# Optimization experiments

Hardware: AMD Instinct MI355X
Metric: run time of the kernel (lower is better)

Reference implementation:

```python
import jax, jax.numpy as jnp
import numpy as np

N = 50000
E = 800000
IN_FEAT = 128
HIDDEN = 64
HEADS = 4
CLASSES = 40
NEG_SLOPE = 0.2


def setup_inputs() -> dict:
    key = jax.random.key(0)
    ks = jax.random.split(key, 12)
    x = jax.random.normal(ks[0], (N, IN_FEAT), dtype=jnp.float32)
    # edge_index without self loops (module removes then re-adds them)
    src = jax.random.randint(ks[1], (E,), 0, N)
    off = jax.random.randint(ks[2], (E,), 1, N)
    dst = (src + off) % N  # guaranteed dst != src
    edge_index = jnp.stack([src, dst]).astype(jnp.int64)
    g = 1.0 / np.sqrt(IN_FEAT)
    lin1_w = jax.random.normal(ks[3], (IN_FEAT, HEADS * HIDDEN), dtype=jnp.float32) * g
    lin1_b = jax.random.normal(ks[4], (HEADS * HIDDEN,), dtype=jnp.float32) * 0.01
    att1 = jax.random.normal(ks[5], (1, HEADS, 2 * HIDDEN), dtype=jnp.float32) * (1.0 / np.sqrt(2 * HIDDEN))
    bias1 = jnp.zeros((HEADS * HIDDEN,), dtype=jnp.float32)
    lin2_w = jax.random.normal(ks[6], (HEADS * HIDDEN, CLASSES), dtype=jnp.float32) * (1.0 / np.sqrt(HEADS * HIDDEN))
    lin2_b = jax.random.normal(ks[7], (CLASSES,), dtype=jnp.float32) * 0.01
    att2 = jax.random.normal(ks[8], (1, 1, 2 * CLASSES), dtype=jnp.float32) * (1.0 / np.sqrt(2 * CLASSES))
    bias2 = jnp.zeros((CLASSES,), dtype=jnp.float32)
    return {"x": x, "edge_index": edge_index, "lin1_w": lin1_w, "lin1_b": lin1_b,
            "att1": att1, "bias1": bias1, "lin2_w": lin2_w, "lin2_b": lin2_b,
            "att2": att2, "bias2": bias2}


def gat_conv(x, src, dst, W, b_lin, att, bias, heads, oc):
    n = x.shape[0]
    fea = (x @ W + b_lin).reshape(n, heads, oc)            # [N, H, C]
    # attention logits: (cat([x_i, x_j]) * att).sum(-1) decomposed per node
    score_i = jnp.einsum('nhc,hc->nh', fea, att[0, :, :oc])  # target half
    score_j = jnp.einsum('nhc,hc->nh', fea, att[0, :, oc:])  # source half
    alpha = score_i[dst] + score_j[src]                    # [E, H]
    alpha = jax.nn.leaky_relu(alpha, NEG_SLOPE)
    # segment softmax over target node
    amax = jax.ops.segment_max(alpha, dst, num_segments=n)
    alpha = jnp.exp(alpha - amax[dst])
    asum = jax.ops.segment_sum(alpha, dst, num_segments=n)
    alpha = alpha / (asum[dst] + 1e-16)
    # message = x_j * alpha; scatter-add to target
    msg = fea[src] * alpha[:, :, None]                     # [E, H, C]
    out = jax.ops.segment_sum(msg, dst, num_segments=n)
    return out.reshape(n, heads * oc) + bias               # concat=True


def reference(x, edge_index, lin1_w, lin1_b, att1, bias1, lin2_w, lin2_b, att2, bias2):
    n = x.shape[0]
    loop = jnp.arange(n, dtype=edge_index.dtype)
    src = jnp.concatenate([edge_index[0], loop])  # add self loops
    dst = jnp.concatenate([edge_index[1], loop])
    h = gat_conv(x, src, dst, lin1_w, lin1_b, att1, bias1, HEADS, HIDDEN)
    h = jax.nn.relu(h)
    h = gat_conv(h, src, dst, lin2_w, lin2_b, att2, bias2, 1, CLASSES)
    return jax.nn.softmax(h, axis=1)
```

## Files before the change

### kernel.cpp

```cpp
#include <hip/hip_runtime.h>
#include <hip/hip_fp16.h>

#define NN 50000
#define NE 800000
#define INFEAT 128
#define F1 256
#define HID 64
#define CLS 40
#define NEGS 0.2f
#define NB 49

__device__ __forceinline__ float lrelu(float x) { return x > 0.0f ? x : NEGS * x; }

struct alignas(8) H4 { __half2 a, b; };
struct alignas(16) H8 { __half2 a, b, c, d; };

typedef __attribute__((ext_vector_type(8))) _Float16 f16x8;
typedef __attribute__((ext_vector_type(4))) float f32x4;

#define GBM 128
__global__ __launch_bounds__(256) void gemm1_k(const float* __restrict__ A,
                                               const float* __restrict__ W,
                                               const float* __restrict__ b,
                                               const float* __restrict__ att1,
                                               __half* __restrict__ feah,
                                               float* __restrict__ sI,
                                               float* __restrict__ sJ) {
    __shared__ __align__(16) _Float16 As[128][40];
    __shared__ __align__(16) _Float16 Ws[64][40];
    int tid = threadIdx.x;
    int wid = tid >> 6, lane = tid & 63;
    int row0 = blockIdx.x * GBM;
    int head = blockIdx.y;
    int colB = head * 64;
    int lr = lane & 15;
    int lg = lane >> 4;

    f32x4 acc[2][4];
    #pragma unroll
    for (int rt = 0; rt < 2; ++rt)
        #pragma unroll
        for (int ct = 0; ct < 4; ++ct) acc[rt][ct] = (f32x4){0.f, 0.f, 0.f, 0.f};

    int wcol = tid & 63;
    int wkg  = tid >> 6;

    for (int k0 = 0; k0 < INFEAT; k0 += 32) {
        #pragma unroll
        for (int i = 0; i < 4; ++i) {
            int q = tid + 256 * i;
            int r = q >> 3;
            int c4 = (q & 7) * 4;
            int grow = row0 + r;
            float4 v = make_float4(0.f, 0.f, 0.f, 0.f);
            if (grow < NN) v = *(const float4*)&A[(size_t)grow * INFEAT + k0 + c4];
            As[r][c4 + 0] = (_Float16)v.x; As[r][c4 + 1] = (_Float16)v.y;
            As[r][c4 + 2] = (_Float16)v.z; As[r][c4 + 3] = (_Float16)v.w;
        }
        {
            f16x8 wv;
            #pragma unroll
            for (int j = 0; j < 8; ++j)
                wv[j] = (_Float16)W[(size_t)(k0 + wkg * 8 + j) * F1 + colB + wcol];
            *(f16x8*)&Ws[wcol][wkg * 8] = wv;
        }
        __syncthreads();
        f16x8 afrag[2], bfrag[4];
        #pragma unroll
        for (int rt = 0; rt < 2; ++rt)
            afrag[rt] = *(const f16x8*)&As[wid * 32 + rt * 16 + lr][lg * 8];
        #pragma unroll
        for (int ct = 0; ct < 4; ++ct)
            bfrag[ct] = *(const f16x8*)&Ws[ct * 16 + lr][lg * 8];
        #pragma unroll
        for (int rt = 0; rt < 2; ++rt)
            #pragma unroll
            for (int ct = 0; ct < 4; ++ct)
                acc[rt][ct] = __builtin_amdgcn_mfma_f32_16x16x32_f16(
                    afrag[rt], bfrag[ct], acc[rt][ct], 0, 0, 0);
        __syncthreads();
    }
    float aIv[4], aJv[4], bv[4];
    #pragma unroll
    for (int ct = 0; ct < 4; ++ct) {
        int cin = ct * 16 + lr;
        aIv[ct] = att1[head * 2 * HID + cin];
        aJv[ct] = att1[head * 2 * HID + HID + cin];
        bv[ct]  = b[colB + cin];
    }
    #pragma unroll
    for (int rt = 0; rt < 2; ++rt) {
        #pragma unroll
        for (int i = 0; i < 4; ++i) {
            int grow = row0 + wid * 32 + rt * 16 + lg * 4 + i;
            float o[4];
            float sIp = 0.f, sJp = 0.f;
            #pragma unroll
            for (int ct = 0; ct < 4; ++ct) {
                o[ct] = acc[rt][ct][i] + bv[ct];
                sIp += o[ct] * aIv[ct];
                sJp += o[ct] * aJv[ct];
            }
            #pragma unroll
            for (int off = 1; off < 16; off <<= 1) {
                sIp += __shfl_xor(sIp, off);
                sJp += __shfl_xor(sJp, off);
            }
            if (grow < NN) {
                #pragma unroll
                for (int ct = 0; ct < 4; ++ct)
                    feah[(size_t)grow * F1 + colB + ct * 16 + lr] = __float2half(o[ct]);
                if (lr == 0) {
                    sI[grow * 4 + head] = sIp;
                    sJ[grow * 4 + head] = sJp;
                }
            }
        }
    }
}

__global__ void hist_k(const int* __restrict__ dst, int* __restrict__ deg,
                       int* __restrict__ ord) {
    int e = blockIdx.x * blockDim.x + threadIdx.x;
    if (e < NE) ord[e] = atomicAdd(&deg[dst[e]], 1);
}

__global__ __launch_bounds__(1024) void scan1_k(const int* __restrict__ deg,
                                                int* __restrict__ row_off,
                                                int* __restrict__ bsum) {
    __shared__ int tmp[1024];
    int tid = threadIdx.x;
    int gid = blockIdx.x * 1024 + tid;
    int v = (gid < NN) ? deg[gid] : 0;
    tmp[tid] = v;
    __syncthreads();
    #pragma unroll
    for (int off = 1; off < 1024; off <<= 1) {
        int t = (tid >= off) ? tmp[tid - off] : 0;
        __syncthreads();
        tmp[tid] += t;
        __syncthreads();
    }
    if (gid < NN) row_off[gid] = tmp[tid] - v;
    if (tid == 1023) bsum[blockIdx.x] = tmp[1023];
}

__global__ void scan2_k(const int* __restrict__ bsum, int* __restrict__ bpref) {
    int tid = threadIdx.x;
    int orig = (tid < NB) ? bsum[tid] : 0;
    int v = orig;
    #pragma unroll
    for (int off = 1; off < 64; off <<= 1) {
        int t = __shfl_up(v, off);
        if (tid >= off) v += t;
    }
    if (tid < NB) bpref[tid] = v - orig;
}

__global__ __launch_bounds__(1024) void scan3_k(int* __restrict__ row_off,
                                                const int* __restrict__ bpref) {
    int gid = blockIdx.x * 1024 + threadIdx.x;
    if (gid < NN) row_off[gid] += bpref[blockIdx.x];
    if (gid == 0) row_off[NN] = NE;
}

__global__ void scatter_k(const int* __restrict__ src, const int* __restrict__ dst,
                          const int* __restrict__ ord, const int* __restrict__ row_off,
                          const float* __restrict__ sI, const float* __restrict__ sJ,
                          int* __restrict__ csr, float4* __restrict__ ep4) {
    int e = blockIdx.x * blockDim.x + threadIdx.x;
    if (e >= NE) return;
    int s = src[e], d = dst[e];
    int pos = row_off[d] + ord[e];
    float4 si = *(const float4*)&sI[d * 4];
    float4 sj = *(const float4*)&sJ[s * 4];
    float4 r;
    r.x = __expf(lrelu(si.x + sj.x));
    r.y = __expf(lrelu(si.y + sj.y));
    r.z = __expf(lrelu(si.z + sj.z));
    r.w = __expf(lrelu(si.w + sj.w));
    csr[pos] = s;
    ep4[pos] = r;
}

__global__ __launch_bounds__(256, 6) void agg1_k(const __half* __restrict__ feah,
                                                 const float* __restrict__ sI,
                                                 const float* __restrict__ sJ,
                                                 const float* __restrict__ epf,
                                                 const int* __restrict__ row_off,
                                                 const int* __restrict__ csr,
                                                 const float* __restrict__ bias,
                                                 float* __restrict__ out) {
    int wid = threadIdx.x >> 6, lane = threadIdx.x & 63;
    int n = blockIdx.x * 4 + wid;
    if (n >= NN) return;
    int h = lane >> 4;
    int c = lane * 4;
    float p = __expf(lrelu(sI[n * 4 + h] + sJ[n * 4 + h]));
    float asum = p;
    H4 vs = *(const H4*)&feah[(size_t)n * F1 + c];
    float2 sx = __half22float2(vs.a), sy = __half22float2(vs.b);
    float4 acc = make_float4(sx.x * p, sx.y * p, sy.x * p, sy.y * p);
    int beg = row_off[n], end = row_off[n + 1];
    int e = beg;
    for (; e + 8 <= end; e += 8) {
        int s0 = csr[e + 0], s1 = csr[e + 1], s2 = csr[e + 2], s3 = csr[e + 3];
        int s4 = csr[e + 4], s5 = csr[e + 5], s6 = csr[e + 6], s7 = csr[e + 7];
        float p0 = epf[(e + 0) * 4 + h], p1 = epf[(e + 1) * 4 + h];
        float p2 = epf[(e + 2) * 4 + h], p3 = epf[(e + 3) * 4 + h];
        float p4 = epf[(e + 4) * 4 + h], p5 = epf[(e + 5) * 4 + h];
        float p6 = epf[(e + 6) * 4 + h], p7 = epf[(e + 7) * 4 + h];
        H4 v0 = *(const H4*)&feah[(size_t)s0 * F1 + c];
        H4 v1 = *(const H4*)&feah[(size_t)s1 * F1 + c];
        H4 v2 = *(const H4*)&feah[(size_t)s2 * F1 + c];
        H4 v3 = *(const H4*)&feah[(size_t)s3 * F1 + c];
        H4 v4 = *(const H4*)&feah[(size_t)s4 * F1 + c];
        H4 v5 = *(const H4*)&feah[(size_t)s5 * F1 + c];
        H4 v6 = *(const H4*)&feah[(size_t)s6 * F1 + c];
        H4 v7 = *(const H4*)&feah[(size_t)s7 * F1 + c];
        asum += ((p0 + p1) + (p2 + p3)) + ((p4 + p5) + (p6 + p7));
        float2 x0 = __half22float2(v0.a), y0 = __half22float2(v0.b);
        float2 x1 = __half22float2(v1.a), y1 = __half22float2(v1.b);
        float2 x2 = __half22float2(v2.a), y2 = __half22float2(v2.b);
        float2 x3 = __half22float2(v3.a), y3 = __half22float2(v3.b);
        float2 x4 = __half22float2(v4.a), y4 = __half22float2(v4.b);
        float2 x5 = __half22float2(v5.a), y5 = __half22float2(v5.b);
        float2 x6 = __half22float2(v6.a), y6 = __half22float2(v6.b);
        float2 x7 = __half22float2(v7.a), y7 = __half22float2(v7.b);
        acc.x += (x0.x * p0 + x1.x * p1 + x2.x * p2 + x3.x * p3)
               + (x4.x * p4 + x5.x * p5 + x6.x * p6 + x7.x * p7);
        acc.y += (x0.y * p0 + x1.y * p1 + x2.y * p2 + x3.y * p3)
               + (x4.y * p4 + x5.y * p5 + x6.y * p6 + x7.y * p7);
        acc.z += (y0.x * p0 + y1.x * p1 + y2.x * p2 + y3.x * p3)
               + (y4.x * p4 + y5.x * p5 + y6.x * p6 + y7.x * p7);
        acc.w += (y0.y * p0 + y1.y * p1 + y2.y * p2 + y3.y * p3)
               + (y4.y * p4 + y5.y * p5 + y6.y * p6 + y7.y * p7);
    }
    for (; e + 4 <= end; e += 4) {
        int s0 = csr[e], s1 = csr[e + 1], s2 = csr[e + 2], s3 = csr[e + 3];
        float p0 = epf[(e + 0) * 4 + h], p1 = epf[(e + 1) * 4 + h];
        float p2 = epf[(e + 2) * 4 + h], p3 = epf[(e + 3) * 4 + h];
        H4 v0 = *(const H4*)&feah[(size_t)s0 * F1 + c];
        H4 v1 = *(const H4*)&feah[(size_t)s1 * F1 + c];
        H4 v2 = *(const H4*)&feah[(size_t)s2 * F1 + c];
        H4 v3 = *(const H4*)&feah[(size_t)s3 * F1 + c];
        asum += (p0 + p1) + (p2 + p3);
        float2 x0 = __half22float2(v0.a), y0 = __half22float2(v0.b);
        float2 x1 = __half22float2(v1.a), y1 = __half22float2(v1.b);
        float2 x2 = __half22float2(v2.a), y2 = __half22float2(v2.b);
        float2 x3 = __half22float2(v3.a), y3 = __half22float2(v3.b);
        acc.x += x0.x * p0 + x1.x * p1 + x2.x * p2 + x3.x * p3;
        acc.y += x0.y * p0 + x1.y * p1 + x2.y * p2 + x3.y * p3;
        acc.z += y0.x * p0 + y1.x * p1 + y2.x * p2 + y3.x * p3;
        acc.w += y0.y * p0 + y1.y * p1 + y2.y * p2 + y3.y * p3;
    }
    for (; e < end; ++e) {
        int s = csr[e];
        float pe = epf[e * 4 + h];
        asum += pe;
        H4 v = *(const H4*)&feah[(size_t)s * F1 + c];
        float2 x = __half22float2(v.a), y = __half22float2(v.b);
        acc.x += x.x * pe; acc.y += x.y * pe;
        acc.z += y.x * pe; acc.w += y.y * pe;
    }
    float inv = 1.0f / (asum + 1e-16f);
    float4 bv = *(const float4*)&bias[c];
    float4 o;
    o.x = fmaxf(acc.x * inv + bv.x, 0.f);
    o.y = fmaxf(acc.y * inv + bv.y, 0.f);
    o.z = fmaxf(acc.z * inv + bv.z, 0.f);
    o.w = fmaxf(acc.w * inv + bv.w, 0.f);
    *(float4*)&out[(size_t)n * F1 + c] = o;
}

#define G2N 102
__global__ __launch_bounds__(256) void gemm2_k(const float* __restrict__ h1,
                                               const float* __restrict__ W2,
                                               const float* __restrict__ b2,
                                               const float* __restrict__ att2,
                                               __half* __restrict__ fea2h,
                                               float* __restrict__ s2I,
                                               float* __restrict__ s2J) {
    __shared__ float Ws[F1 * CLS];
    __shared__ float redI[G2N][5];
    __shared__ float redJ[G2N][5];
    int tid = threadIdx.x;
    for (int i = tid * 4; i < F1 * CLS; i += 256 * 4)
        *(float4*)&Ws[i] = *(const float4*)&W2[i];
    __syncthreads();
    int nl = tid / 5, g = tid - nl * 5;
    int na = blockIdx.x * G2N + nl * 2;
    int nb = na + 1;
    bool actA = (tid < 255) && (na < NN);
    bool actB = (tid < 255) && (nb < NN);
    int c0 = g * 8;
    float accA[8] = {}, accB[8] = {};
    if (actA) {
        const float* rowA = h1 + (size_t)na * F1;
        const float* rowB = h1 + (size_t)(actB ? nb : na) * F1;
        for (int k = 0; k < F1; k += 4) {
            float4 ha = *(const float4*)&rowA[k];
            float4 hb = *(const float4*)&rowB[k];
            float a[4] = {ha.x, ha.y, ha.z, ha.w};
            float bl[4] = {hb.x, hb.y, hb.z, hb.w};
            #pragma unroll
            for (int kk = 0; kk < 4; ++kk) {
                float4 w0 = *(const float4*)&Ws[(k + kk) * CLS + c0];
                float4 w1 = *(const float4*)&Ws[(k + kk) * CLS + c0 + 4];
                accA[0] += a[kk] * w0.x; accA[1] += a[kk] * w0.y;
                accA[2] += a[kk] * w0.z; accA[3] += a[kk] * w0.w;
                accA[4] += a[kk] * w1.x; accA[5] += a[kk] * w1.y;
                accA[6] += a[kk] * w1.z; accA[7] += a[kk] * w1.w;
                accB[0] += bl[kk] * w0.x; accB[1] += bl[kk] * w0.y;
                accB[2] += bl[kk] * w0.z; accB[3] += bl[kk] * w0.w;
                accB[4] += bl[kk] * w1.x; accB[5] += bl[kk] * w1.y;
                accB[6] += bl[kk] * w1.z; accB[7] += bl[kk] * w1.w;
            }
        }
        float4 bb0 = *(const float4*)&b2[c0];
        float4 bb1 = *(const float4*)&b2[c0 + 4];
        float bias8[8] = {bb0.x, bb0.y, bb0.z, bb0.w, bb1.x, bb1.y, bb1.z, bb1.w};
        float sIa = 0.f, sJa = 0.f, sIb = 0.f, sJb = 0.f;
        #pragma unroll
        for (int j = 0; j < 8; ++j) {
            accA[j] += bias8[j];
            accB[j] += bias8[j];
            float aI = att2[c0 + j], aJ = att2[CLS + c0 + j];
            sIa += accA[j] * aI; sJa += accA[j] * aJ;
            sIb += accB[j] * aI; sJb += accB[j] * aJ;
        }
        H8 ha8;
        ha8.a = __floats2half2_rn(accA[0], accA[1]);
        ha8.b = __floats2half2_rn(accA[2], accA[3]);
        ha8.c = __floats2half2_rn(accA[4], accA[5]);
        ha8.d = __floats2half2_rn(accA[6], accA[7]);
        *(H8*)&fea2h[(size_t)na * CLS + c0] = ha8;
        redI[nl * 2][g] = sIa;
        redJ[nl * 2][g] = sJa;
        if (actB) {
            H8 hb8;
            hb8.a = __floats2half2_rn(accB[0], accB[1]);
            hb8.b = __floats2half2_rn(accB[2], accB[3]);
            hb8.c = __floats2half2_rn(accB[4], accB[5]);
            hb8.d = __floats2half2_rn(accB[6], accB[7]);
            *(H8*)&fea2h[(size_t)nb * CLS + c0] = hb8;
            redI[nl * 2 + 1][g] = sIb;
            redJ[nl * 2 + 1][g] = sJb;
        }
    }
    __syncthreads();
    if (actA && g == 0) {
        int r = nl * 2;
        s2I[na] = redI[r][0] + redI[r][1] + redI[r][2] + redI[r][3] + redI[r][4];
        s2J[na] = redJ[r][0] + redJ[r][1] + redJ[r][2] + redJ[r][3] + redJ[r][4];
        if (actB) {
            s2I[nb] = redI[r + 1][0] + redI[r + 1][1] + redI[r + 1][2] + redI[r + 1][3] + redI[r + 1][4];
            s2J[nb] = redJ[r + 1][0] + redJ[r + 1][1] + redJ[r + 1][2] + redJ[r + 1][3] + redJ[r + 1][4];
        }
    }
}

__global__ __launch_bounds__(256) void agg2_k(const __half* __restrict__ fea2h,
                                              const float* __restrict__ s2I,
                                              const float* __restrict__ s2J,
                                              const int* __restrict__ row_off,
                                              const int* __restrict__ csr,
                                              const float* __restrict__ bias2,
                                              float* __restrict__ out) {
    int wid = threadIdx.x >> 6, lane = threadIdx.x & 63;
    int n = blockIdx.x * 4 + wid;
    if (n >= NN) return;
    float si = s2I[n], sjn = s2J[n];
    int c = lane < CLS ? lane : 0;
    float p = __expf(lrelu(si + sjn));
    float asum = p;
    float acc = __half2float(fea2h[(size_t)n * CLS + c]) * p;
    int beg = row_off[n], end = row_off[n + 1];
    int e = beg;
    for (; e + 8 <= end; e += 8) {
        int s0 = csr[e + 0], s1 = csr[e + 1], s2 = csr[e + 2], s3 = csr[e + 3];
        int s4 = csr[e + 4], s5 = csr[e + 5], s6 = csr[e + 6], s7 = csr[e + 7];
        float a0 = s2J[s0], a1 = s2J[s1], a2 = s2J[s2], a3 = s2J[s3];
        float a4 = s2J[s4], a5 = s2J[s5], a6 = s2J[s6], a7 = s2J[s7];
        __half f0 = fea2h[(size_t)s0 * CLS + c];
        __half f1 = fea2h[(size_t)s1 * CLS + c];
        __half f2 = fea2h[(size_t)s2 * CLS + c];
        __half f3 = fea2h[(size_t)s3 * CLS + c];
        __half f4 = fea2h[(size_t)s4 * CLS + c];
        __half f5 = fea2h[(size_t)s5 * CLS + c];
        __half f6 = fea2h[(size_t)s6 * CLS + c];
        __half f7 = fea2h[(size_t)s7 * CLS + c];
        float p0 = __expf(lrelu(si + a0));
        float p1 = __expf(lrelu(si + a1));
        float p2 = __expf(lrelu(si + a2));
        float p3 = __expf(lrelu(si + a3));
        float p4 = __expf(lrelu(si + a4));
        float p5 = __expf(lrelu(si + a5));
        float p6 = __expf(lrelu(si + a6));
        float p7 = __expf(lrelu(si + a7));
        asum += ((p0 + p1) + (p2 + p3)) + ((p4 + p5) + (p6 + p7));
        acc += (__half2float(f0) * p0 + __half2float(f1) * p1
              + __half2float(f2) * p2 + __half2float(f3) * p3)
             + (__half2float(f4) * p4 + __half2float(f5) * p5
              + __half2float(f6) * p6 + __half2float(f7) * p7);
    }
    for (; e + 4 <= end; e += 4) {
        int s0 = csr[e], s1 = csr[e + 1], s2 = csr[e + 2], s3 = csr[e + 3];
        float p0 = __expf(lrelu(si + s2J[s0]));
        float p1 = __expf(lrelu(si + s2J[s1]));
        float p2 = __expf(lrelu(si + s2J[s2]));
        float p3 = __expf(lrelu(si + s2J[s3]));
        __half f0 = fea2h[(size_t)s0 * CLS + c];
        __half f1 = fea2h[(size_t)s1 * CLS + c];
        __half f2 = fea2h[(size_t)s2 * CLS + c];
        __half f3 = fea2h[(size_t)s3 * CLS + c];
        asum += (p0 + p1) + (p2 + p3);
        acc += __half2float(f0) * p0 + __half2float(f1) * p1
             + __half2float(f2) * p2 + __half2float(f3) * p3;
    }
    for (; e < end; ++e) {
        int s = csr[e];
        float pe = __expf(lrelu(si + s2J[s]));
        asum += pe;
        acc += __half2float(fea2h[(size_t)s * CLS + c]) * pe;
    }
    float row = acc / (asum + 1e-16f) + bias2[c];
    float v = (lane < CLS) ? row : -3.0e38f;
    float vm = v;
    #pragma unroll
    for (int off = 32; off; off >>= 1) vm = fmaxf(vm, __shfl_xor(vm, off));
    float ex = (lane < CLS) ? __expf(v - vm) : 0.f;
    float es = ex;
    #pragma unroll
    for (int off = 32; off; off >>= 1) es += __shfl_xor(es, off);
    if (lane < CLS) out[(size_t)n * CLS + lane] = ex / es;
}

extern "C" void kernel_launch(void* const* d_in, const int* in_sizes, int n_in,
                              void* d_out, int out_size, void* d_ws, size_t ws_size,
                              hipStream_t stream) {
    const float* x     = (const float*)d_in[0];
    const int*   ei    = (const int*)d_in[1];
    const float* w1    = (const float*)d_in[2];
    const float* b1    = (const float*)d_in[3];
    const float* att1  = (const float*)d_in[4];
    const float* bias1 = (const float*)d_in[5];
    const float* w2    = (const float*)d_in[6];
    const float* b2    = (const float*)d_in[7];
    const float* att2  = (const float*)d_in[8];
    const float* bias2 = (const float*)d_in[9];
    const int* src = ei;
    const int* dst = ei + NE;
    float* out = (float*)d_out;

    char* p = (char*)d_ws;
    auto alloc = [&](size_t bytes) {
        char* r = p;
        p += (bytes + 255) & ~(size_t)255;
        return r;
    };
    __half* fea1h = (__half*)alloc((size_t)NN * F1 * 2);
    float* h1     = (float*)alloc((size_t)NN * F1 * 4);
    float* sI1    = (float*)alloc((size_t)NN * 4 * 4);
    float* sJ1    = (float*)alloc((size_t)NN * 4 * 4);
    __half* fea2h = (__half*)alloc((size_t)NN * CLS * 2);
    float* s2I    = (float*)alloc((size_t)NN * 4);
    float* s2J    = (float*)alloc((size_t)NN * 4);
    int*   deg    = (int*)alloc((size_t)NN * 4);
    int*   row_off= (int*)alloc((size_t)(NN + 1) * 4);
    int*   bsum   = (int*)alloc((size_t)NB * 4);
    int*   bpref  = (int*)alloc((size_t)NB * 4);
    int*   ord    = (int*)alloc((size_t)NE * 4);
    int*   csr    = (int*)alloc((size_t)NE * 4);
    float* ep1    = (float*)alloc((size_t)NE * 4 * 4);

    hipMemsetAsync(deg, 0, (size_t)NN * 4, stream);

    dim3 g1((NN + GBM - 1) / GBM, 4);
    gemm1_k<<<g1, 256, 0, stream>>>(x, w1, b1, att1, fea1h, sI1, sJ1);
    hist_k<<<(NE + 255) / 256, 256, 0, stream>>>(dst, deg, ord);
    scan1_k<<<NB, 1024, 0, stream>>>(deg, row_off, bsum);
    scan2_k<<<1, 64, 0, stream>>>(bsum, bpref);
    scan3_k<<<NB, 1024, 0, stream>>>(row_off, bpref);
    scatter_k<<<(NE + 255) / 256, 256, 0, stream>>>(src, dst, ord, row_off,
                                                    sI1, sJ1, csr, (float4*)ep1);
    agg1_k<<<(NN + 3) / 4, 256, 0, stream>>>(fea1h, sI1, sJ1, ep1, row_off, csr, bias1, h1);
    gemm2_k<<<(NN + G2N - 1) / G2N, 256, 0, stream>>>(h1, w2, b2, att2, fea2h, s2I, s2J);
    agg2_k<<<(NN + 3) / 4, 256, 0, stream>>>(fea2h, s2I, s2J, row_off, csr, bias2, out);
}
```

Before: 228.4 us.

## Store layer-1 output in fp16 and compute second GEMM with MFMA

The first aggregation kernel now writes its ReLU output as fp16 instead of fp32, halving the intermediate buffer traffic. The second linear layer is rewritten as an MFMA 16x16x32 f16 kernel with 128-row tiles, an fp16 transposed weight tile padded to 48 columns, and shuffle-based reduction for the attention scores. This replaces the scalar FMA loop over fp32 shared weights. It adds fp16 rounding of the hidden activations and padded work on 8 dummy columns.

Result: no change. 224.2 us (-1.8%).

```diff
diff --git a/kernel.cpp b/kernel.cpp
--- a/kernel.cpp
+++ b/kernel.cpp
@@ -190,7 +190,7 @@
                                                  const int* __restrict__ row_off,
                                                  const int* __restrict__ csr,
                                                  const float* __restrict__ bias,
-                                                 float* __restrict__ out) {
+                                                 __half* __restrict__ out) {
     int wid = threadIdx.x >> 6, lane = threadIdx.x & 63;
     int n = blockIdx.x * 4 + wid;
     if (n >= NN) return;
@@ -265,97 +265,115 @@
     }
     float inv = 1.0f / (asum + 1e-16f);
     float4 bv = *(const float4*)&bias[c];
-    float4 o;
-    o.x = fmaxf(acc.x * inv + bv.x, 0.f);
-    o.y = fmaxf(acc.y * inv + bv.y, 0.f);
-    o.z = fmaxf(acc.z * inv + bv.z, 0.f);
-    o.w = fmaxf(acc.w * inv + bv.w, 0.f);
-    *(float4*)&out[(size_t)n * F1 + c] = o;
-}
-
-#define G2N 102
-__global__ __launch_bounds__(256) void gemm2_k(const float* __restrict__ h1,
+    H4 o4;
+    o4.a = __floats2half2_rn(fmaxf(acc.x * inv + bv.x, 0.f),
+                             fmaxf(acc.y * inv + bv.y, 0.f));
+    o4.b = __floats2half2_rn(fmaxf(acc.z * inv + bv.z, 0.f),
+                             fmaxf(acc.w * inv + bv.w, 0.f));
+    *(H4*)&out[(size_t)n * F1 + c] = o4;
+}
+
+#define G2M 128
+__global__ __launch_bounds__(256) void gemm2_k(const __half* __restrict__ h1h,
                                                const float* __restrict__ W2,
                                                const float* __restrict__ b2,
                                                const float* __restrict__ att2,
                                                __half* __restrict__ fea2h,
                                                float* __restrict__ s2I,
                                                float* __restrict__ s2J) {
-    __shared__ float Ws[F1 * CLS];
-    __shared__ float redI[G2N][5];
-    __shared__ float redJ[G2N][5];
+    __shared__ __align__(16) _Float16 Ws2[48][264];
+    __shared__ __align__(16) _Float16 As2[128][40];
     int tid = threadIdx.x;
-    for (int i = tid * 4; i < F1 * CLS; i += 256 * 4)
-        *(float4*)&Ws[i] = *(const float4*)&W2[i];
-    __syncthreads();
-    int nl = tid / 5, g = tid - nl * 5;
-    int na = blockIdx.x * G2N + nl * 2;
-    int nb = na + 1;
-    bool actA = (tid < 255) && (na < NN);
-    bool actB = (tid < 255) && (nb < NN);
-    int c0 = g * 8;
-    float accA[8] = {}, accB[8] = {};
-    if (actA) {
-        const float* rowA = h1 + (size_t)na * F1;
-        const float* rowB = h1 + (size_t)(actB ? nb : na) * F1;
-        for (int k = 0; k < F1; k += 4) {
-            float4 ha = *(const float4*)&rowA[k];
-            float4 hb = *(const float4*)&rowB[k];
-            float a[4] = {ha.x, ha.y, ha.z, ha.w};
-            float bl[4] = {hb.x, hb.y, hb.z, hb.w};
-            #pragma unroll
-            for (int kk = 0; kk < 4; ++kk) {
-                float4 w0 = *(const float4*)&Ws[(k + kk) * CLS + c0];
-                float4 w1 = *(const float4*)&Ws[(k + kk) * CLS + c0 + 4];
-                accA[0] += a[kk] * w0.x; accA[1] += a[kk] * w0.y;
-                accA[2] += a[kk] * w0.z; accA[3] += a[kk] * w0.w;
-                accA[4] += a[kk] * w1.x; accA[5] += a[kk] * w1.y;
-                accA[6] += a[kk] * w1.z; accA[7] += a[kk] * w1.w;
-                accB[0] += bl[kk] * w0.x; accB[1] += bl[kk] * w0.y;
-                accB[2] += bl[kk] * w0.z; accB[3] += bl[kk] * w0.w;
-                accB[4] += bl[kk] * w1.x; accB[5] += bl[kk] * w1.y;
-                accB[6] += bl[kk] * w1.z; accB[7] += bl[kk] * w1.w;
-            }
+    int wid = tid >> 6, lane = tid & 63;
+    int lr = lane & 15, lg = lane >> 4;
+    int row0 = blockIdx.x * G2M;
+    for (int q = tid; q < 48 * 32; q += 256) {
+        int col = q >> 5;
+        int kg  = q & 31;
+        f16x8 wv;
+        #pragma unroll
+        for (int j = 0; j < 8; ++j) {
+            int k = kg * 8 + j;
+            wv[j] = (col < CLS) ? (_Float16)W2[(size_t)k * CLS + col] : (_Float16)0.f;
         }
-        float4 bb0 = *(const float4*)&b2[c0];
-        float4 bb1 = *(const float4*)&b2[c0 + 4];
-        float bias8[8] = {bb0.x, bb0.y, bb0.z, bb0.w, bb1.x, bb1.y, bb1.z, bb1.w};
-        float sIa = 0.f, sJa = 0.f, sIb = 0.f, sJb = 0.f;
-        #pragma unroll
-        for (int j = 0; j < 8; ++j) {
-            accA[j] += bias8[j];
-            accB[j] += bias8[j];
-            float aI = att2[c0 + j], aJ = att2[CLS + c0 + j];
-            sIa += accA[j] * aI; sJa += accA[j] * aJ;
-            sIb += accB[j] * aI; sJb += accB[j] * aJ;
+        *(f16x8*)&Ws2[col][kg * 8] = wv;
+    }
+    f32x4 acc[2][3];
+    #pragma unroll
+    for (int rt = 0; rt < 2; ++rt)
+        #pragma unroll
+        for (int ct = 0; ct < 3; ++ct) acc[rt][ct] = (f32x4){0.f, 0.f, 0.f, 0.f};
+
+    for (int k0 = 0; k0 < F1; k0 += 32) {
+        #pragma unroll
+        for (int i = 0; i < 2; ++i) {
+            int q = tid + 256 * i;
+            int r = q >> 2;
+            int c8 = (q & 3) * 8;
+            int grow = row0 + r;
+            f16x8 v;
+            if (grow < NN) v = *(const f16x8*)&h1h[(size_t)grow * F1 + k0 + c8];
+            else {
+                #pragma unroll
+                for (int j = 0; j < 8; ++j) v[j] = (_Float16)0.f;
+            }
+            *(f16x8*)&As2[r][c8] = v;
         }
-        H8 ha8;
-        ha8.a = __floats2half2_rn(accA[0], accA[1]);
-        ha8.b = __floats2half2_rn(accA[2], accA[3]);
-        ha8.c = __floats2half2_rn(accA[4], accA[5]);
-        ha8.d = __floats2half2_rn(accA[6], accA[7]);
-        *(H8*)&fea2h[(size_t)na * CLS + c0] = ha8;
-        redI[nl * 2][g] = sIa;
-        redJ[nl * 2][g] = sJa;
-        if (actB) {
-            H8 hb8;
-            hb8.a = __floats2half2_rn(accB[0], accB[1]);
-            hb8.b = __floats2half2_rn(accB[2], accB[3]);
-            hb8.c = __floats2half2_rn(accB[4], accB[5]);
-            hb8.d = __floats2half2_rn(accB[6], accB[7]);
-            *(H8*)&fea2h[(size_t)nb * CLS + c0] = hb8;
-            redI[nl * 2 + 1][g] = sIb;
-            redJ[nl * 2 + 1][g] = sJb;
-        }
-    }
-    __syncthreads();
-    if (actA && g == 0) {
-        int r = nl * 2;
-        s2I[na] = redI[r][0] + redI[r][1] + redI[r][2] + redI[r][3] + redI[r][4];
-        s2J[na] = redJ[r][0] + redJ[r][1] + redJ[r][2] + redJ[r][3] + redJ[r][4];
-        if (actB) {
-            s2I[nb] = redI[r + 1][0] + redI[r + 1][1] + redI[r + 1][2] + redI[r + 1][3] + redI[r + 1][4];
-            s2J[nb] = redJ[r + 1][0] + redJ[r + 1][1] + redJ[r + 1][2] + redJ[r + 1][3] + redJ[r + 1][4];
+        __syncthreads();
+        f16x8 af[2], bf[3];
+        #pragma unroll
+        for (int rt = 0; rt < 2; ++rt)
+            af[rt] = *(const f16x8*)&As2[wid * 32 + rt * 16 + lr][lg * 8];
+        #pragma unroll
+        for (int ct = 0; ct < 3; ++ct)
+            bf[ct] = *(const f16x8*)&Ws2[ct * 16 + lr][k0 + lg * 8];
+        #pragma unroll
+        for (int rt = 0; rt < 2; ++rt)
+            #pragma unroll
+            for (int ct = 0; ct < 3; ++ct)
+                acc[rt][ct] = __builtin_amdgcn_mfma_f32_16x16x32_f16(
+                    af[rt], bf[ct], acc[rt][ct], 0, 0, 0);
+        __syncthreads();
+    }
+    float bcol[3], aIc[3], aJc[3];
+    bool valid[3];
+    #pragma unroll
+    for (int ct = 0; ct < 3; ++ct) {
+        int col = ct * 16 + lr;
+        valid[ct] = col < CLS;
+        int cc = valid[ct] ? col : 0;
+        bcol[ct] = b2[cc];
+        aIc[ct] = valid[ct] ? att2[cc] : 0.f;
+        aJc[ct] = valid[ct] ? att2[CLS + cc] : 0.f;
+    }
+    #pragma unroll
+    for (int rt = 0; rt < 2; ++rt) {
+        #pragma unroll
+        for (int i = 0; i < 4; ++i) {
+            int grow = row0 + wid * 32 + rt * 16 + lg * 4 + i;
+            float o[3];
+            float sIp = 0.f, sJp = 0.f;
+            #pragma unroll
+            for (int ct = 0; ct < 3; ++ct) {
+                o[ct] = acc[rt][ct][i] + bcol[ct];
+                sIp += o[ct] * aIc[ct];
+                sJp += o[ct] * aJc[ct];
+            }
+            #pragma unroll
+            for (int off = 1; off < 16; off <<= 1) {
+                sIp += __shfl_xor(sIp, off);
+                sJp += __shfl_xor(sJp, off);
+            }
+            if (grow < NN) {
+                #pragma unroll
+                for (int ct = 0; ct < 3; ++ct)
+                    if (valid[ct])
+                        fea2h[(size_t)grow * CLS + ct * 16 + lr] = __float2half(o[ct]);
+                if (lr == 0) {
+                    s2I[grow] = sIp;
+                    s2J[grow] = sJp;
+                }
+            }
         }
     }
 }
@@ -460,7 +478,7 @@
         return r;
     };
     __half* fea1h = (__half*)alloc((size_t)NN * F1 * 2);
-    float* h1     = (float*)alloc((size_t)NN * F1 * 4);
+    __half* h1h   = (__half*)alloc((size_t)NN * F1 * 2);
     float* sI1    = (float*)alloc((size_t)NN * 4 * 4);
     float* sJ1    = (float*)alloc((size_t)NN * 4 * 4);
     __half* fea2h = (__half*)alloc((size_t)NN * CLS * 2);
@@ -484,7 +502,7 @@
     scan3_k<<<NB, 1024, 0, stream>>>(row_off, bpref);
     scatter_k<<<(NE + 255) / 256, 256, 0, stream>>>(src, dst, ord, row_off,
                                                     sI1, sJ1, csr, (float4*)ep1);
-    agg1_k<<<(NN + 3) / 4, 256, 0, stream>>>(fea1h, sI1, sJ1, ep1, row_off, csr, bias1, h1);
-    gemm2_k<<<(NN + G2N - 1) / G2N, 256, 0, stream>>>(h1, w2, b2, att2, fea2h, s2I, s2J);
+    agg1_k<<<(NN + 3) / 4, 256, 0, stream>>>(fea1h, sI1, sJ1, ep1, row_off, csr, bias1, h1h);
+    gemm2_k<<<(NN + G2M - 1) / G2M, 256, 0, stream>>>(h1h, w2, b2, att2, fea2h, s2I, s2J);
     agg2_k<<<(NN + 3) / 4, 256, 0, stream>>>(fea2h, s2I, s2J, row_off, csr, bias2, out);
 }
```
